# Kernel optimization log

Measured on AMD Instinct MI355X. Metric: run time of the kernel, lower is better.

Reference implementation:

```python
import jax, jax.numpy as jnp
import numpy as np

R = 128  # num_regions
F = 128  # num_features
K = 4    # num_gaussian_kernels


def setup_inputs() -> dict:
    key = jax.random.key(0)
    k1, k2, k3, k4, k5 = jax.random.split(key, 5)
    N = 128
    x1 = jax.random.normal(k1, (N, R * F), dtype=jnp.float32)
    x2 = jax.random.normal(k2, (N, R * F), dtype=jnp.float32)
    # per-kernel learned scalars: sigma ~ randn*100, mean ~ randn
    sigmas = jax.random.normal(k3, (K,), dtype=jnp.float32) * 100.0
    means = jax.random.normal(k4, (K,), dtype=jnp.float32)
    # CustomModel.sigma_parameters ~ randn(K); weights = 1/sigma_parameters**2
    sigma_params = jax.random.normal(k5, (K,), dtype=jnp.float32)
    return {"x1": x1, "x2": x2, "sigmas": sigmas, "means": means,
            "sigma_params": sigma_params}


def reference(x1, x2, sigmas, means, sigma_params):
    N = x1.shape[0]
    a = x1.reshape(N, R, F)
    b = x2.reshape(N, R, F)
    # ||a_i - b_j - m||^2 = ||a_i - b_j||^2 - 2*m*sum(a_i - b_j) + F*m^2
    # expand the pairwise squared distance to avoid the (N,R,R,F) tensor
    dot = jnp.einsum('nif,njf->nij', a, b)                     # (N,R,R)
    sq = (jnp.sum(a * a, -1)[:, :, None]
          + jnp.sum(b * b, -1)[:, None, :] - 2.0 * dot)        # (N,R,R)
    lin = jnp.sum(a, -1)[:, :, None] - jnp.sum(b, -1)[:, None, :]  # (N,R,R)
    m = means[:, None, None, None]                             # (K,1,1,1)
    sg = sigmas[:, None, None, None]
    d2 = sq[None] - 2.0 * m * lin[None] + F * m * m            # (K,N,R,R)
    kernel_value = jnp.exp(-d2 / (2.0 * sg * sg))
    sim = jax.nn.softmax(kernel_value, axis=-1)                # softmax over j
    w = jax.nn.softmax(1.0 / (sigma_params * sigma_params))    # (K,)
    return jnp.einsum('k,knij->nij', w, sim)                   # (N,R,R)
```

## Files before the change

kernel.cpp:

```cpp
#include <hip/hip_runtime.h>

#define N_BATCH 128
#define R_DIM 128
#define F_DIM 128

__global__ __launch_bounds__(512, 2) void kmix_kernel(
    const float* __restrict__ x1,
    const float* __restrict__ x2,
    const float* __restrict__ sigmas,
    const float* __restrict__ means,
    const float* __restrict__ sigma_params,
    float* __restrict__ out)
{
    constexpr float LOG2E = 1.4426950408889634f;
    const int t   = threadIdx.x;
    const int lp  = t & 31;
    const int grp = t >> 5;
    const int n     = blockIdx.x >> 1;
    const int ibase = (blockIdx.x & 1) << 6;

    __shared__ __align__(16) float As[F_DIM * 64];
    __shared__ __align__(16) float Bs[F_DIM * 128];
    __shared__ __align__(16) float rbS[128];
    __shared__ __align__(16) float sbS[128];

    const float* Ag = x1 + (size_t)n * (R_DIM * F_DIM) + (size_t)ibase * F_DIM;
    const float* Bg = x2 + (size_t)n * (R_DIM * F_DIM);

    const int sw4 = (lp & 7) << 2;

    #pragma unroll
    for (int s = 0; s < 8; ++s) {
        const int j = grp + (s << 4);
        const float4 v = *(const float4*)(Bg + j * F_DIM + (lp << 2));
        const int jsw = j ^ sw4;
        Bs[(lp * 4 + 0) * 128 + jsw] = v.x;
        Bs[(lp * 4 + 1) * 128 + jsw] = v.y;
        Bs[(lp * 4 + 2) * 128 + jsw] = v.z;
        Bs[(lp * 4 + 3) * 128 + jsw] = v.w;
        float s1 = v.x + v.y + v.z + v.w;
        float s2 = v.x * v.x + v.y * v.y + v.z * v.z + v.w * v.w;
        #pragma unroll
        for (int m = 16; m >= 1; m >>= 1) {
            s1 += __shfl_xor(s1, m, 64);
            s2 += __shfl_xor(s2, m, 64);
        }
        if (lp == 0) { sbS[j] = s1; rbS[j] = s2; }
    }

    #pragma unroll
    for (int s = 0; s < 4; ++s) {
        const int i = grp + (s << 4);
        const float4 v = *(const float4*)(Ag + i * F_DIM + (lp << 2));
        const int isw = i ^ sw4;
        As[(lp * 4 + 0) * 64 + isw] = v.x;
        As[(lp * 4 + 1) * 64 + isw] = v.y;
        As[(lp * 4 + 2) * 64 + isw] = v.z;
        As[(lp * 4 + 3) * 64 + isw] = v.w;
    }

    __syncthreads();

    float acc[4][4] = {};
    const float4* A4 = (const float4*)As;
    const float4* B4 = (const float4*)Bs;
    #pragma unroll 4
    for (int f = 0; f < F_DIM; ++f) {
        const int sw = (f >> 2) & 7;
        const float4 av = A4[f * 16 + (grp ^ sw)];
        const float4 bv = B4[f * 32 + (lp  ^ sw)];
        const float a0 = av.x, a1 = av.y, a2 = av.z, a3 = av.w;
        const float b0 = bv.x, b1 = bv.y, b2 = bv.z, b3 = bv.w;
        acc[0][0] = fmaf(a0, b0, acc[0][0]); acc[0][1] = fmaf(a0, b1, acc[0][1]);
        acc[0][2] = fmaf(a0, b2, acc[0][2]); acc[0][3] = fmaf(a0, b3, acc[0][3]);
        acc[1][0] = fmaf(a1, b0, acc[1][0]); acc[1][1] = fmaf(a1, b1, acc[1][1]);
        acc[1][2] = fmaf(a1, b2, acc[1][2]); acc[1][3] = fmaf(a1, b3, acc[1][3]);
        acc[2][0] = fmaf(a2, b0, acc[2][0]); acc[2][1] = fmaf(a2, b1, acc[2][1]);
        acc[2][2] = fmaf(a2, b2, acc[2][2]); acc[2][3] = fmaf(a2, b3, acc[2][3]);
        acc[3][0] = fmaf(a3, b0, acc[3][0]); acc[3][1] = fmaf(a3, b1, acc[3][1]);
        acc[3][2] = fmaf(a3, b2, acc[3][2]); acc[3][3] = fmaf(a3, b3, acc[3][3]);
    }

    const float4 rb4 = *(const float4*)(rbS + (lp << 2));
    const float4 sb4 = *(const float4*)(sbS + (lp << 2));

    float sg[4], mn[4], tk[4];
    #pragma unroll
    for (int k = 0; k < 4; ++k) {
        sg[k] = sigmas[k];
        mn[k] = means[k];
        const float spv = sigma_params[k];
        tk[k] = 1.0f / (spv * spv);
    }
    const float tmax = fmaxf(fmaxf(tk[0], tk[1]), fmaxf(tk[2], tk[3]));
    float wk[4]; float wsum = 0.0f;
    #pragma unroll
    for (int k = 0; k < 4; ++k) {
        wk[k] = __builtin_amdgcn_exp2f((tk[k] - tmax) * LOG2E);
        wsum += wk[k];
    }
    const float winv = 1.0f / wsum;

    float oacc[4][4] = {};
    #pragma unroll
    for (int k = 0; k < 4; ++k) {
        const float inv = 1.0f / (sg[k] * sg[k]);
        const float cD =  LOG2E * inv;
        const float cA = -0.5f * LOG2E * inv;
        const float cB = -LOG2E * mn[k] * inv;
        float q[4];
        q[0] = fmaf(cA, rb4.x, cB * sb4.x);
        q[1] = fmaf(cA, rb4.y, cB * sb4.y);
        q[2] = fmaf(cA, rb4.z, cB * sb4.z);
        q[3] = fmaf(cA, rb4.w, cB * sb4.w);
        const float wkn = wk[k] * winv;
        #pragma unroll
        for (int r = 0; r < 4; ++r) {
            float sc0 = fmaf(cD, acc[r][0], q[0]);
            float sc1 = fmaf(cD, acc[r][1], q[1]);
            float sc2 = fmaf(cD, acc[r][2], q[2]);
            float sc3 = fmaf(cD, acc[r][3], q[3]);
            float mx = fmaxf(fmaxf(sc0, sc1), fmaxf(sc2, sc3));
            #pragma unroll
            for (int m = 16; m >= 1; m >>= 1)
                mx = fmaxf(mx, __shfl_xor(mx, m, 64));
            const float e0 = __builtin_amdgcn_exp2f(sc0 - mx);
            const float e1 = __builtin_amdgcn_exp2f(sc1 - mx);
            const float e2 = __builtin_amdgcn_exp2f(sc2 - mx);
            const float e3 = __builtin_amdgcn_exp2f(sc3 - mx);
            float ss = e0 + e1 + e2 + e3;
            #pragma unroll
            for (int m = 16; m >= 1; m >>= 1)
                ss += __shfl_xor(ss, m, 64);
            const float scale = wkn * __builtin_amdgcn_rcpf(ss);
            oacc[r][0] = fmaf(scale, e0, oacc[r][0]);
            oacc[r][1] = fmaf(scale, e1, oacc[r][1]);
            oacc[r][2] = fmaf(scale, e2, oacc[r][2]);
            oacc[r][3] = fmaf(scale, e3, oacc[r][3]);
        }
    }

    float* O = out + (size_t)n * (R_DIM * R_DIM) + (size_t)ibase * R_DIM + (lp << 2);
    #pragma unroll
    for (int r = 0; r < 4; ++r) {
        const float4 v = make_float4(oacc[r][0], oacc[r][1], oacc[r][2], oacc[r][3]);
        *(float4*)(O + (grp * 4 + r) * R_DIM) = v;
    }
}

extern "C" void kernel_launch(void* const* d_in, const int* in_sizes, int n_in,
                              void* d_out, int out_size, void* d_ws, size_t ws_size,
                              hipStream_t stream) {
    const float* x1 = (const float*)d_in[0];
    const float* x2 = (const float*)d_in[1];
    const float* sigmas = (const float*)d_in[2];
    const float* means = (const float*)d_in[3];
    const float* sigma_params = (const float*)d_in[4];
    float* out = (float*)d_out;
    dim3 grid(N_BATCH * 2), block(512);
    hipLaunchKernelGGL(kmix_kernel, grid, block, 0, stream,
                       x1, x2, sigmas, means, sigma_params, out);
}
```

Before: 88.57 us.

## Compute batched dot products with split-fp16 MFMA and cross-wave softmax merge

```diff
diff --git a/kernel.cpp b/kernel.cpp
--- a/kernel.cpp
+++ b/kernel.cpp
@@ -1,99 +1,122 @@
 #include <hip/hip_runtime.h>
 
-#define N_BATCH 128
-#define R_DIM 128
-#define F_DIM 128
-
-__global__ __launch_bounds__(512, 2) void kmix_kernel(
-    const float* __restrict__ x1,
-    const float* __restrict__ x2,
-    const float* __restrict__ sigmas,
-    const float* __restrict__ means,
-    const float* __restrict__ sigma_params,
-    float* __restrict__ out)
+#define LOG2E 1.4426950408889634f
+
+typedef _Float16 half8 __attribute__((ext_vector_type(8)));
+typedef float floatx4 __attribute__((ext_vector_type(4)));
+
+__global__ __launch_bounds__(512, 2) void kmix_mfma(
+    const float* __restrict__ x1, const float* __restrict__ x2,
+    const float* __restrict__ sigmas, const float* __restrict__ means,
+    const float* __restrict__ sigma_params, float* __restrict__ out)
 {
-    constexpr float LOG2E = 1.4426950408889634f;
-    const int t   = threadIdx.x;
-    const int lp  = t & 31;
-    const int grp = t >> 5;
+    const int t    = threadIdx.x;
+    const int lane = t & 63;
+    const int w    = t >> 6;
+    const int it   = w >> 1;
+    const int jh   = w & 1;
     const int n     = blockIdx.x >> 1;
     const int ibase = (blockIdx.x & 1) << 6;
 
-    __shared__ __align__(16) float As[F_DIM * 64];
-    __shared__ __align__(16) float Bs[F_DIM * 128];
-    __shared__ __align__(16) float rbS[128];
-    __shared__ __align__(16) float sbS[128];
-
-    const float* Ag = x1 + (size_t)n * (R_DIM * F_DIM) + (size_t)ibase * F_DIM;
-    const float* Bg = x2 + (size_t)n * (R_DIM * F_DIM);
-
-    const int sw4 = (lp & 7) << 2;
-
-    #pragma unroll
-    for (int s = 0; s < 8; ++s) {
-        const int j = grp + (s << 4);
-        const float4 v = *(const float4*)(Bg + j * F_DIM + (lp << 2));
-        const int jsw = j ^ sw4;
-        Bs[(lp * 4 + 0) * 128 + jsw] = v.x;
-        Bs[(lp * 4 + 1) * 128 + jsw] = v.y;
-        Bs[(lp * 4 + 2) * 128 + jsw] = v.z;
-        Bs[(lp * 4 + 3) * 128 + jsw] = v.w;
-        float s1 = v.x + v.y + v.z + v.w;
-        float s2 = v.x * v.x + v.y * v.y + v.z * v.z + v.w * v.w;
-        #pragma unroll
-        for (int m = 16; m >= 1; m >>= 1) {
-            s1 += __shfl_xor(s1, m, 64);
-            s2 += __shfl_xor(s2, m, 64);
-        }
-        if (lp == 0) { sbS[j] = s1; rbS[j] = s2; }
+    __shared__ half8 BhS[32][64];
+    __shared__ half8 BlS[32][64];
+    __shared__ float rbS[128], sbS[128];
+    __shared__ float exM[4][4][2][16];
+    __shared__ float exS[4][4][2][16];
+
+    const float* Ag = x1 + (size_t)n * 16384 + (size_t)ibase * 128;
+    const float* Bg = x2 + (size_t)n * 16384;
+
+    const int am = lane & 15;
+    const int aq = lane >> 4;
+
+    const float* arow = Ag + (it * 16 + am) * 128 + aq * 8;
+    float4 a0[4], a1[4];
+    #pragma unroll
+    for (int ks = 0; ks < 4; ++ks) {
+        a0[ks] = *(const float4*)(arow + ks * 32);
+        a1[ks] = *(const float4*)(arow + ks * 32 + 4);
     }
 
     #pragma unroll
     for (int s = 0; s < 4; ++s) {
-        const int i = grp + (s << 4);
-        const float4 v = *(const float4*)(Ag + i * F_DIM + (lp << 2));
-        const int isw = i ^ sw4;
-        As[(lp * 4 + 0) * 64 + isw] = v.x;
-        As[(lp * 4 + 1) * 64 + isw] = v.y;
-        As[(lp * 4 + 2) * 64 + isw] = v.z;
-        As[(lp * 4 + 3) * 64 + isw] = v.w;
+        const int frag = s * 8 + w;
+        const int slot = lane;
+        const int j = (frag >> 2) * 16 + (slot & 15);
+        const int c = (frag & 3) * 4 + (slot >> 4);
+        const float* p = Bg + j * 128 + c * 8;
+        const float4 v0 = ((const float4*)p)[0];
+        const float4 v1 = ((const float4*)p)[1];
+        const float vv[8] = {v0.x, v0.y, v0.z, v0.w, v1.x, v1.y, v1.z, v1.w};
+        half8 h, l;
+        #pragma unroll
+        for (int e = 0; e < 8; ++e) {
+            const _Float16 hv = (_Float16)vv[e];
+            h[e] = hv;
+            l[e] = (_Float16)(vv[e] - (float)hv);
+        }
+        BhS[frag][slot] = h;
+        BlS[frag][slot] = l;
+    }
+
+    {
+        const int j  = t >> 2;
+        const int qq = t & 3;
+        const float* p = Bg + j * 128 + qq * 32;
+        float s1 = 0.f, s2 = 0.f;
+        #pragma unroll
+        for (int c = 0; c < 8; ++c) {
+            const float4 v = ((const float4*)p)[c];
+            s1 += v.x + v.y + v.z + v.w;
+            s2 += v.x * v.x + v.y * v.y + v.z * v.z + v.w * v.w;
+        }
+        s1 += __shfl_xor(s1, 1); s2 += __shfl_xor(s2, 1);
+        s1 += __shfl_xor(s1, 2); s2 += __shfl_xor(s2, 2);
+        if (qq == 0) { sbS[j] = s1; rbS[j] = s2; }
+    }
+
+    half8 Ah[4], Al[4];
+    #pragma unroll
+    for (int ks = 0; ks < 4; ++ks) {
+        const float av[8] = {a0[ks].x, a0[ks].y, a0[ks].z, a0[ks].w,
+                             a1[ks].x, a1[ks].y, a1[ks].z, a1[ks].w};
+        #pragma unroll
+        for (int e = 0; e < 8; ++e) {
+            const _Float16 hv = (_Float16)av[e];
+            Ah[ks][e] = hv;
+            Al[ks][e] = (_Float16)(av[e] - (float)hv);
+        }
     }
 
     __syncthreads();
 
-    float acc[4][4] = {};
-    const float4* A4 = (const float4*)As;
-    const float4* B4 = (const float4*)Bs;
-    #pragma unroll 4
-    for (int f = 0; f < F_DIM; ++f) {
-        const int sw = (f >> 2) & 7;
-        const float4 av = A4[f * 16 + (grp ^ sw)];
-        const float4 bv = B4[f * 32 + (lp  ^ sw)];
-        const float a0 = av.x, a1 = av.y, a2 = av.z, a3 = av.w;
-        const float b0 = bv.x, b1 = bv.y, b2 = bv.z, b3 = bv.w;
-        acc[0][0] = fmaf(a0, b0, acc[0][0]); acc[0][1] = fmaf(a0, b1, acc[0][1]);
-        acc[0][2] = fmaf(a0, b2, acc[0][2]); acc[0][3] = fmaf(a0, b3, acc[0][3]);
-        acc[1][0] = fmaf(a1, b0, acc[1][0]); acc[1][1] = fmaf(a1, b1, acc[1][1]);
-        acc[1][2] = fmaf(a1, b2, acc[1][2]); acc[1][3] = fmaf(a1, b3, acc[1][3]);
-        acc[2][0] = fmaf(a2, b0, acc[2][0]); acc[2][1] = fmaf(a2, b1, acc[2][1]);
-        acc[2][2] = fmaf(a2, b2, acc[2][2]); acc[2][3] = fmaf(a2, b3, acc[2][3]);
-        acc[3][0] = fmaf(a3, b0, acc[3][0]); acc[3][1] = fmaf(a3, b1, acc[3][1]);
-        acc[3][2] = fmaf(a3, b2, acc[3][2]); acc[3][3] = fmaf(a3, b3, acc[3][3]);
-    }
-
-    const float4 rb4 = *(const float4*)(rbS + (lp << 2));
-    const float4 sb4 = *(const float4*)(sbS + (lp << 2));
-
-    float sg[4], mn[4], tk[4];
-    #pragma unroll
-    for (int k = 0; k < 4; ++k) {
-        sg[k] = sigmas[k];
-        mn[k] = means[k];
+    floatx4 acc[4] = {};
+    #pragma unroll
+    for (int ks = 0; ks < 4; ++ks) {
+        #pragma unroll
+        for (int jt = 0; jt < 4; ++jt) {
+            const int frag = (jh * 4 + jt) * 4 + ks;
+            const half8 bh = BhS[frag][lane];
+            const half8 bl = BlS[frag][lane];
+            acc[jt] = __builtin_amdgcn_mfma_f32_16x16x32_f16(Ah[ks], bh, acc[jt], 0, 0, 0);
+            acc[jt] = __builtin_amdgcn_mfma_f32_16x16x32_f16(Al[ks], bh, acc[jt], 0, 0, 0);
+            acc[jt] = __builtin_amdgcn_mfma_f32_16x16x32_f16(Ah[ks], bl, acc[jt], 0, 0, 0);
+        }
+    }
+
+    float cD[4], cA[4], cB[4], wk[4], tk[4];
+    #pragma unroll
+    for (int k = 0; k < 4; ++k) {
+        const float sgv = sigmas[k];
+        const float inv = 1.0f / (sgv * sgv);
+        cD[k] = LOG2E * inv;
+        cA[k] = -0.5f * LOG2E * inv;
+        cB[k] = -LOG2E * means[k] * inv;
         const float spv = sigma_params[k];
         tk[k] = 1.0f / (spv * spv);
     }
     const float tmax = fmaxf(fmaxf(tk[0], tk[1]), fmaxf(tk[2], tk[3]));
-    float wk[4]; float wsum = 0.0f;
+    float wsum = 0.f;
     #pragma unroll
     for (int k = 0; k < 4; ++k) {
         wk[k] = __builtin_amdgcn_exp2f((tk[k] - tmax) * LOG2E);
@@ -101,50 +124,80 @@
     }
     const float winv = 1.0f / wsum;
 
+    float rbv[4], sbv[4];
+    #pragma unroll
+    for (int jt = 0; jt < 4; ++jt) {
+        const int j = jh * 64 + jt * 16 + am;
+        rbv[jt] = rbS[j];
+        sbv[jt] = sbS[j];
+    }
+
+    float eK[4][4][4];
+    float mW[4][4], sW[4][4];
+    #pragma unroll
+    for (int k = 0; k < 4; ++k) {
+        float sc[4][4];
+        #pragma unroll
+        for (int jt = 0; jt < 4; ++jt) {
+            const float qv = fmaf(cA[k], rbv[jt], cB[k] * sbv[jt]);
+            #pragma unroll
+            for (int r = 0; r < 4; ++r)
+                sc[jt][r] = fmaf(cD[k], acc[jt][r], qv);
+        }
+        #pragma unroll
+        for (int r = 0; r < 4; ++r) {
+            float m = fmaxf(fmaxf(sc[0][r], sc[1][r]), fmaxf(sc[2][r], sc[3][r]));
+            m = fmaxf(m, __shfl_xor(m, 1));
+            m = fmaxf(m, __shfl_xor(m, 2));
+            m = fmaxf(m, __shfl_xor(m, 4));
+            m = fmaxf(m, __shfl_xor(m, 8));
+            float ssum = 0.f;
+            #pragma unroll
+            for (int jt = 0; jt < 4; ++jt) {
+                const float e = __builtin_amdgcn_exp2f(sc[jt][r] - m);
+                eK[k][jt][r] = e;
+                ssum += e;
+            }
+            ssum += __shfl_xor(ssum, 1);
+            ssum += __shfl_xor(ssum, 2);
+            ssum += __shfl_xor(ssum, 4);
+            ssum += __shfl_xor(ssum, 8);
+            mW[k][r] = m;
+            sW[k][r] = ssum;
+            if (am == 0) {
+                exM[k][it][jh][aq * 4 + r] = m;
+                exS[k][it][jh][aq * 4 + r] = ssum;
+            }
+        }
+    }
+    __syncthreads();
+
     float oacc[4][4] = {};
     #pragma unroll
     for (int k = 0; k < 4; ++k) {
-        const float inv = 1.0f / (sg[k] * sg[k]);
-        const float cD =  LOG2E * inv;
-        const float cA = -0.5f * LOG2E * inv;
-        const float cB = -LOG2E * mn[k] * inv;
-        float q[4];
-        q[0] = fmaf(cA, rb4.x, cB * sb4.x);
-        q[1] = fmaf(cA, rb4.y, cB * sb4.y);
-        q[2] = fmaf(cA, rb4.z, cB * sb4.z);
-        q[3] = fmaf(cA, rb4.w, cB * sb4.w);
         const float wkn = wk[k] * winv;
         #pragma unroll
         for (int r = 0; r < 4; ++r) {
-            float sc0 = fmaf(cD, acc[r][0], q[0]);
-            float sc1 = fmaf(cD, acc[r][1], q[1]);
-            float sc2 = fmaf(cD, acc[r][2], q[2]);
-            float sc3 = fmaf(cD, acc[r][3], q[3]);
-            float mx = fmaxf(fmaxf(sc0, sc1), fmaxf(sc2, sc3));
+            const float mo = exM[k][it][jh ^ 1][aq * 4 + r];
+            const float so = exS[k][it][jh ^ 1][aq * 4 + r];
+            const float M  = fmaxf(mW[k][r], mo);
+            const float dw = __builtin_amdgcn_exp2f(mW[k][r] - M);
+            const float do_ = __builtin_amdgcn_exp2f(mo - M);
+            const float S  = fmaf(sW[k][r], dw, so * do_);
+            const float scale = wkn * dw * __builtin_amdgcn_rcpf(S);
             #pragma unroll
-            for (int m = 16; m >= 1; m >>= 1)
-                mx = fmaxf(mx, __shfl_xor(mx, m, 64));
-            const float e0 = __builtin_amdgcn_exp2f(sc0 - mx);
-            const float e1 = __builtin_amdgcn_exp2f(sc1 - mx);
-            const float e2 = __builtin_amdgcn_exp2f(sc2 - mx);
-            const float e3 = __builtin_amdgcn_exp2f(sc3 - mx);
-            float ss = e0 + e1 + e2 + e3;
-            #pragma unroll
-            for (int m = 16; m >= 1; m >>= 1)
-                ss += __shfl_xor(ss, m, 64);
-            const float scale = wkn * __builtin_amdgcn_rcpf(ss);
-            oacc[r][0] = fmaf(scale, e0, oacc[r][0]);
-            oacc[r][1] = fmaf(scale, e1, oacc[r][1]);
-            oacc[r][2] = fmaf(scale, e2, oacc[r][2]);
-            oacc[r][3] = fmaf(scale, e3, oacc[r][3]);
-        }
-    }
-
-    float* O = out + (size_t)n * (R_DIM * R_DIM) + (size_t)ibase * R_DIM + (lp << 2);
+            for (int jt = 0; jt < 4; ++jt)
+                oacc[jt][r] = fmaf(scale, eK[k][jt][r], oacc[jt][r]);
+        }
+    }
+
+    float* O = out + (size_t)n * 16384 + (size_t)(ibase + it * 16 + aq * 4) * 128
+             + jh * 64 + am;
     #pragma unroll
     for (int r = 0; r < 4; ++r) {
-        const float4 v = make_float4(oacc[r][0], oacc[r][1], oacc[r][2], oacc[r][3]);
-        *(float4*)(O + (grp * 4 + r) * R_DIM) = v;
+        #pragma unroll
+        for (int jt = 0; jt < 4; ++jt)
+            O[r * 128 + jt * 16] = oacc[jt][r];
     }
 }
 
@@ -157,7 +210,6 @@
     const float* means = (const float*)d_in[3];
     const float* sigma_params = (const float*)d_in[4];
     float* out = (float*)d_out;
-    dim3 grid(N_BATCH * 2), block(512);
-    hipLaunchKernelGGL(kmix_kernel, grid, block, 0, stream,
+    hipLaunchKernelGGL(kmix_mfma, dim3(256), dim3(512), 0, stream,
                        x1, x2, sigmas, means, sigma_params, out);
 }
```

Measured after the change: 86.57 us. 1.02x faster.
